# Kernel tuning notes

Measured on AMD Instinct MI355X. Metric: run time of the kernel, lower is better.

Reference implementation:

```python
import jax, jax.numpy as jnp
import numpy as np

D_MODEL = 2048
NUM_Q_HEADS = 32
NUM_KV_HEADS = 8
HEAD_DIM = D_MODEL // NUM_Q_HEADS  # 64
NUM_GROUPS = NUM_Q_HEADS // NUM_KV_HEADS  # 4
SCALE = float(np.sqrt(HEAD_DIM))


def setup_inputs() -> dict:
    key = jax.random.key(0)
    ks = jax.random.split(key, 5)
    B, S = 2, 2048
    std = 1.0 / np.sqrt(D_MODEL)
    return {
        "x": jax.random.normal(ks[0], (B, S, D_MODEL), dtype=jnp.float32),
        "W_q": jax.random.normal(ks[1], (D_MODEL, NUM_Q_HEADS * HEAD_DIM), dtype=jnp.float32) * std,
        "W_k": jax.random.normal(ks[2], (D_MODEL, NUM_KV_HEADS * HEAD_DIM), dtype=jnp.float32) * std,
        "W_v": jax.random.normal(ks[3], (D_MODEL, NUM_KV_HEADS * HEAD_DIM), dtype=jnp.float32) * std,
        "W_o": jax.random.normal(ks[4], (D_MODEL, D_MODEL), dtype=jnp.float32) * std,
    }


def reference(x, W_q, W_k, W_v, W_o):
    B, S, _ = x.shape
    # projections; weights stored as (in, out) so y = x @ W
    Q = (x @ W_q).reshape(B, S, NUM_Q_HEADS, HEAD_DIM).transpose(0, 2, 1, 3)   # [B,Hq,S,d]
    K = (x @ W_k).reshape(B, S, NUM_KV_HEADS, HEAD_DIM).transpose(0, 2, 1, 3)  # [B,Hkv,S,d]
    V = (x @ W_v).reshape(B, S, NUM_KV_HEADS, HEAD_DIM).transpose(0, 2, 1, 3)
    # repeat_interleave KV heads across groups (faithful to the original)
    K = jnp.repeat(K, NUM_GROUPS, axis=1)  # [B,Hq,S,d]
    V = jnp.repeat(V, NUM_GROUPS, axis=1)
    scores = jnp.einsum("bhqd,bhkd->bhqk", Q, K) / SCALE  # [B,Hq,S,S]
    attn = jax.nn.softmax(scores, axis=-1)
    out = jnp.einsum("bhqk,bhkd->bhqd", attn, V)  # [B,Hq,S,d]
    out = out.transpose(0, 2, 1, 3).reshape(B, S, D_MODEL)
    return out @ W_o
```

## Files before the change

### kernel.cpp

```cpp
#include <hip/hip_runtime.h>
#include <hip/hip_bf16.h>

#define D_MODEL 2048
#define NQH 32
#define NKVH 8
#define HD 64
#define SEQ 2048
#define BATCH 2
#define MTOT (BATCH * SEQ)

typedef __attribute__((ext_vector_type(8))) short short8;
typedef __attribute__((ext_vector_type(4))) float floatx4;
typedef __attribute__((ext_vector_type(16))) float f32x16;

#define QSCALE 0.18033688011112042f

static __device__ inline unsigned cvtpk(float lo, float hi) {
  unsigned r;
  asm("v_cvt_pk_bf16_f32 %0, %1, %2" : "=v"(r) : "v"(lo), "v"(hi));
  return r;
}
#define PLSWAP(a, b) asm("v_permlane32_swap_b32 %0, %1" : "+v"(a), "+v"(b))

__device__ inline void gload_lds16(const __hip_bfloat16* g, short* lds) {
  __builtin_amdgcn_global_load_lds(
      (const __attribute__((address_space(1))) void*)g,
      (__attribute__((address_space(3))) void*)lds, 16, 0, 0);
}

__global__ __launch_bounds__(256) void convx_k(const float* __restrict__ x,
                                               __hip_bfloat16* __restrict__ xb,
                                               int n4) {
  int i = blockIdx.x * 256 + threadIdx.x;
  int stride = gridDim.x * 256;
  for (; i < n4; i += stride) {
    float4 v = reinterpret_cast<const float4*>(x)[i];
    union { __hip_bfloat16 h[4]; uint2 u; } cv;
    cv.h[0] = __float2bfloat16(v.x);
    cv.h[1] = __float2bfloat16(v.y);
    cv.h[2] = __float2bfloat16(v.z);
    cv.h[3] = __float2bfloat16(v.w);
    reinterpret_cast<uint2*>(xb)[i] = cv.u;
  }
}

__global__ __launch_bounds__(256) void transw_k(const float* __restrict__ W,
                                                __hip_bfloat16* __restrict__ Wt,
                                                int Kd, int Nd) {
  __shared__ float t[32][33];
  int n0 = blockIdx.x * 32, k0 = blockIdx.y * 32;
  int tx = threadIdx.x, ty = threadIdx.y;
#pragma unroll
  for (int j = 0; j < 32; j += 8)
    t[ty + j][tx] = W[(size_t)(k0 + ty + j) * Nd + n0 + tx];
  __syncthreads();
#pragma unroll
  for (int j = 0; j < 32; j += 8)
    Wt[(size_t)(n0 + ty + j) * Kd + k0 + tx] = __float2bfloat16(t[tx][ty + j]);
}

template <int MODE>
__global__ __launch_bounds__(256) void gemm_bt_k(
    const __hip_bfloat16* __restrict__ A,
    const __hip_bfloat16* __restrict__ B0,
    const __hip_bfloat16* __restrict__ B1,
    const __hip_bfloat16* __restrict__ B2,
    float* __restrict__ Cf,
    __hip_bfloat16* __restrict__ O0,
    __hip_bfloat16* __restrict__ O1,
    __hip_bfloat16* __restrict__ O2) {
  constexpr int Kd = D_MODEL;
  __shared__ short As[128 * 32];
  __shared__ short Bs[128 * 32];

  const int tid = threadIdx.x;
  const int m0 = blockIdx.y * 128;
  const int n0 = blockIdx.x * 128;

  const __hip_bfloat16* Bt;
  if (MODE == 0) {
    Bt = B0 + (size_t)n0 * Kd;
  } else {
    if (n0 < 2048) Bt = B0 + (size_t)n0 * Kd;
    else if (n0 < 2560) Bt = B1 + (size_t)(n0 - 2048) * Kd;
    else Bt = B2 + (size_t)(n0 - 2560) * Kd;
  }
  const __hip_bfloat16* Ab = A + (size_t)m0 * Kd;

  const int w = tid >> 6, l = tid & 63;
  const int wr = w >> 1, wc = w & 1;
  const int lc = l & 15, l4 = l >> 4;

  const int srow = w * 32 + (l >> 2);
  const int scol = (l & 3) * 8;
  const __hip_bfloat16* ga = Ab + (size_t)srow * Kd + scol;
  const __hip_bfloat16* gb = Bt + (size_t)srow * Kd + scol;
  short* la0 = &As[(w * 32) * 32];
  short* la1 = &As[(w * 32 + 16) * 32];
  short* lb0 = &Bs[(w * 32) * 32];
  short* lb1 = &Bs[(w * 32 + 16) * 32];

  floatx4 acc[4][4] = {};

  for (int kt = 0; kt < Kd; kt += 32) {
    gload_lds16(ga + kt, la0);
    gload_lds16(ga + (size_t)16 * Kd + kt, la1);
    gload_lds16(gb + kt, lb0);
    gload_lds16(gb + (size_t)16 * Kd + kt, lb1);
    __syncthreads();

    short8 af[4], bf[4];
#pragma unroll
    for (int mi = 0; mi < 4; ++mi)
      af[mi] = *reinterpret_cast<const short8*>(&As[(wr * 64 + mi * 16 + lc) * 32 + l4 * 8]);
#pragma unroll
    for (int ni = 0; ni < 4; ++ni)
      bf[ni] = *reinterpret_cast<const short8*>(&Bs[(wc * 64 + ni * 16 + lc) * 32 + l4 * 8]);
#pragma unroll
    for (int mi = 0; mi < 4; ++mi)
#pragma unroll
      for (int ni = 0; ni < 4; ++ni)
        acc[mi][ni] = __builtin_amdgcn_mfma_f32_16x16x32_bf16(af[mi], bf[ni], acc[mi][ni], 0, 0, 0);
    __syncthreads();
  }

#pragma unroll
  for (int mi = 0; mi < 4; ++mi)
#pragma unroll
    for (int ni = 0; ni < 4; ++ni)
#pragma unroll
      for (int i = 0; i < 4; ++i) {
        int m = m0 + wr * 64 + mi * 16 + l4 * 4 + i;
        int ncol = n0 + wc * 64 + ni * 16 + lc;
        float v = acc[mi][ni][i];
        if (MODE == 0) {
          Cf[(size_t)m * 2048 + ncol] = v;
        } else {
          int bb = m >> 11, s = m & 2047;
          if (ncol < 2048) {
            int hh = ncol >> 6, dd = ncol & 63;
            O0[(((size_t)bb * NQH + hh) * SEQ + s) * HD + dd] = __float2bfloat16(v * QSCALE);
          } else if (ncol < 2560) {
            int c2 = ncol - 2048;
            int hh = c2 >> 6, dd = c2 & 63;
            O1[(((size_t)bb * NKVH + hh) * SEQ + s) * HD + dd] = __float2bfloat16(v);
          } else {
            int c2 = ncol - 2560;
            int hh = c2 >> 6, dd = c2 & 63;
            O2[(((size_t)bb * NKVH + hh) * HD + dd) * SEQ + s] = __float2bfloat16(v);
          }
        }
      }
}

__global__ __launch_bounds__(256, 2) void attn_k(const __hip_bfloat16* __restrict__ Qb,
                                                 const __hip_bfloat16* __restrict__ Kb,
                                                 const __hip_bfloat16* __restrict__ Vtb,
                                                 __hip_bfloat16* __restrict__ Ao) {
  __shared__ short Ks[2][64 * 64];
  __shared__ short Vs[2][64 * 64];
  __shared__ float Ls[4][64];

  const int bid = blockIdx.x;
  const int xcd = bid & 7, j = bid >> 3;
  const int g = xcd * 2 + (j >> 5), wv = j & 31;
  const int b = g >> 3, kh = g & 7;
  const int h = kh * 4 + (wv >> 3), qt = wv & 7;

  const int tid = threadIdx.x, w = tid >> 6, l = tid & 63;
  const int q5 = l & 31, hl = l >> 5;

  const __hip_bfloat16* Qp = Qb + (((size_t)b * NQH + h) * SEQ + qt * 256 + w * 64) * HD;
  const __hip_bfloat16* Kp = Kb + ((size_t)b * NKVH + kh) * SEQ * HD;
  const __hip_bfloat16* Vp = Vtb + ((size_t)b * NKVH + kh) * HD * SEQ;

  short8 qf[2][4];
#pragma unroll
  for (int qb_ = 0; qb_ < 2; ++qb_)
#pragma unroll
    for (int ks = 0; ks < 4; ++ks)
      qf[qb_][ks] = *reinterpret_cast<const short8*>(
          Qp + (size_t)(qb_ * 32 + q5) * HD + ks * 16 + hl * 8);

  f32x16 acc[2][2] = {};
  float lsum[2] = {0.f, 0.f};

  const int sr = w * 8 + (l >> 3);
  const int sc = (l & 7) ^ (sr & 7);

  gload_lds16(Kp + (size_t)sr * HD + sc * 8, &Ks[0][w * 512]);
  gload_lds16(Kp + (size_t)(sr + 32) * HD + sc * 8, &Ks[0][2048 + w * 512]);
  gload_lds16(Vp + (size_t)sr * SEQ + sc * 8, &Vs[0][w * 512]);
  gload_lds16(Vp + (size_t)(sr + 32) * SEQ + sc * 8, &Vs[0][2048 + w * 512]);
  __syncthreads();

  int buf = 0;
  for (int kb = 0; kb < SEQ / 64; ++kb) {
    if (kb < SEQ / 64 - 1) {
      const __hip_bfloat16* Kn = Kp + (size_t)(kb + 1) * 64 * HD;
      const __hip_bfloat16* Vn = Vp + (size_t)(kb + 1) * 64;
      gload_lds16(Kn + (size_t)sr * HD + sc * 8, &Ks[buf ^ 1][w * 512]);
      gload_lds16(Kn + (size_t)(sr + 32) * HD + sc * 8, &Ks[buf ^ 1][2048 + w * 512]);
      gload_lds16(Vn + (size_t)sr * SEQ + sc * 8, &Vs[buf ^ 1][w * 512]);
      gload_lds16(Vn + (size_t)(sr + 32) * SEQ + sc * 8, &Vs[buf ^ 1][2048 + w * 512]);
    }

    const short* Kt = Ks[buf];
    const short* Vt = Vs[buf];

    short8 kf[2][4], vf[2][4];
#pragma unroll
    for (int kblk = 0; kblk < 2; ++kblk)
#pragma unroll
      for (int ks = 0; ks < 4; ++ks) {
        int row = kblk * 32 + q5;
        int ch = (ks * 2 + hl) ^ (row & 7);
        kf[kblk][ks] = *reinterpret_cast<const short8*>(Kt + row * 64 + ch * 8);
      }
#pragma unroll
    for (int db = 0; db < 2; ++db)
#pragma unroll
      for (int t = 0; t < 4; ++t) {
        int row = db * 32 + q5;
        int ch = (t * 2 + hl) ^ (row & 7);
        vf[db][t] = *reinterpret_cast<const short8*>(Vt + row * 64 + ch * 8);
      }

#pragma unroll
    for (int qb_ = 0; qb_ < 2; ++qb_) {
      f32x16 st0 = {}, st1 = {};
      __builtin_amdgcn_s_setprio(1);
#pragma unroll
      for (int ks = 0; ks < 4; ++ks) {
        st0 = __builtin_amdgcn_mfma_f32_32x32x16_bf16(kf[0][ks], qf[qb_][ks], st0, 0, 0, 0);
        st1 = __builtin_amdgcn_mfma_f32_32x32x16_bf16(kf[1][ks], qf[qb_][ks], st1, 0, 0, 0);
      }
      __builtin_amdgcn_s_setprio(0);

      float ps = 0.f;
      unsigned u[2][8];
#pragma unroll
      for (int jj = 0; jj < 8; ++jj) {
        float e0 = exp2f(st0[2 * jj]), e1 = exp2f(st0[2 * jj + 1]);
        float f0 = exp2f(st1[2 * jj]), f1 = exp2f(st1[2 * jj + 1]);
        ps += (e0 + e1) + (f0 + f1);
        u[0][jj] = cvtpk(e0, e1);
        u[1][jj] = cvtpk(f0, f1);
      }
      lsum[qb_] += ps;

      PLSWAP(u[0][0], u[0][2]); PLSWAP(u[0][1], u[0][3]);
      PLSWAP(u[0][4], u[0][6]); PLSWAP(u[0][5], u[0][7]);
      PLSWAP(u[1][0], u[1][2]); PLSWAP(u[1][1], u[1][3]);
      PLSWAP(u[1][4], u[1][6]); PLSWAP(u[1][5], u[1][7]);

      __builtin_amdgcn_s_setprio(1);
#pragma unroll
      for (int t = 0; t < 4; ++t) {
        union { unsigned w4[4]; short8 s8; } pa;
        pa.w4[0] = u[t >> 1][(t & 1) * 4 + 0];
        pa.w4[1] = u[t >> 1][(t & 1) * 4 + 1];
        pa.w4[2] = u[t >> 1][(t & 1) * 4 + 2];
        pa.w4[3] = u[t >> 1][(t & 1) * 4 + 3];
        acc[qb_][0] = __builtin_amdgcn_mfma_f32_32x32x16_bf16(pa.s8, vf[0][t], acc[qb_][0], 0, 0, 0);
        acc[qb_][1] = __builtin_amdgcn_mfma_f32_32x32x16_bf16(pa.s8, vf[1][t], acc[qb_][1], 0, 0, 0);
      }
      __builtin_amdgcn_s_setprio(0);
    }
    __syncthreads();
    buf ^= 1;
  }

#pragma unroll
  for (int qb_ = 0; qb_ < 2; ++qb_) {
    float v = lsum[qb_];
    v += __shfl_xor(v, 32);
    if (l < 32) Ls[w][qb_ * 32 + l] = v;
  }
  __syncthreads();

  const size_t obase = (size_t)b * SEQ + qt * 256 + w * 64;
#pragma unroll
  for (int qb_ = 0; qb_ < 2; ++qb_) {
    float inv[16];
#pragma unroll
    for (int r = 0; r < 16; ++r)
      inv[r] = 1.0f / Ls[w][qb_ * 32 + (r & 3) + 8 * (r >> 2) + 4 * hl];
#pragma unroll
    for (int db = 0; db < 2; ++db)
#pragma unroll
      for (int r = 0; r < 16; ++r) {
        int q = qb_ * 32 + (r & 3) + 8 * (r >> 2) + 4 * hl;
        Ao[(obase + q) * D_MODEL + h * HD + db * 32 + q5] =
            __float2bfloat16(acc[qb_][db][r] * inv[r]);
      }
  }
}

extern "C" void kernel_launch(void* const* d_in, const int* in_sizes, int n_in,
                              void* d_out, int out_size, void* d_ws, size_t ws_size,
                              hipStream_t stream) {
  const float* x  = (const float*)d_in[0];
  const float* Wq = (const float*)d_in[1];
  const float* Wk = (const float*)d_in[2];
  const float* Wv = (const float*)d_in[3];
  const float* Wo = (const float*)d_in[4];
  float* out = (float*)d_out;

  __hip_bfloat16* p = (__hip_bfloat16*)d_ws;
  __hip_bfloat16* xb  = p;
  __hip_bfloat16* Wqt = xb  + (size_t)MTOT * D_MODEL;
  __hip_bfloat16* Wkt = Wqt + (size_t)D_MODEL * D_MODEL;
  __hip_bfloat16* Wvt = Wkt + (size_t)512 * D_MODEL;
  __hip_bfloat16* Wot = Wvt + (size_t)512 * D_MODEL;
  __hip_bfloat16* Qb  = Wot + (size_t)D_MODEL * D_MODEL;
  __hip_bfloat16* Kb  = Qb  + (size_t)MTOT * D_MODEL;
  __hip_bfloat16* Vtb = Kb  + (size_t)BATCH * NKVH * SEQ * HD;
  __hip_bfloat16* Ab  = Vtb + (size_t)BATCH * NKVH * SEQ * HD;

  convx_k<<<2048, 256, 0, stream>>>(x, xb, MTOT * D_MODEL / 4);
  transw_k<<<dim3(D_MODEL / 32, D_MODEL / 32), dim3(32, 8), 0, stream>>>(Wq, Wqt, D_MODEL, D_MODEL);
  transw_k<<<dim3(512 / 32, D_MODEL / 32), dim3(32, 8), 0, stream>>>(Wk, Wkt, D_MODEL, 512);
  transw_k<<<dim3(512 / 32, D_MODEL / 32), dim3(32, 8), 0, stream>>>(Wv, Wvt, D_MODEL, 512);
  transw_k<<<dim3(D_MODEL / 32, D_MODEL / 32), dim3(32, 8), 0, stream>>>(Wo, Wot, D_MODEL, D_MODEL);

  gemm_bt_k<1><<<dim3(24, MTOT / 128), 256, 0, stream>>>(xb, Wqt, Wkt, Wvt,
                                                         nullptr, Qb, Kb, Vtb);
  attn_k<<<dim3(512), 256, 0, stream>>>(Qb, Kb, Vtb, Ab);
  gemm_bt_k<0><<<dim3(D_MODEL / 128, MTOT / 128), 256, 0, stream>>>(Ab, Wot, nullptr, nullptr,
                                                                    out, nullptr, nullptr, nullptr);
}
```

Baseline: 255.1 us.

## Halve attention query tile per wave, double grid, raise occupancy, re-layout LDS

The attention kernel now gives each wave 32 query rows instead of 64. The grid doubles to 1024 blocks and launch bounds go from 2 to 4 blocks per CU, so more waves are available to hide latency. K/V tiles in LDS move from an XOR-swizzled row layout to a chunk-major layout, so fragment reads stay conflict-free without the swizzle. The next-tile prefetch and the V fragment loads are moved after the QK MFMAs and the exp work, to overlap them with compute. The cost is that each K/V tile is reused by half as many queries, which doubles K/V global and LDS traffic per unit of work, and the global loads are less coalesced.

```diff
diff --git a/kernel.cpp b/kernel.cpp
--- a/kernel.cpp
+++ b/kernel.cpp
@@ -153,147 +153,132 @@
       }
 }
 
-__global__ __launch_bounds__(256, 2) void attn_k(const __hip_bfloat16* __restrict__ Qb,
+__global__ __launch_bounds__(256, 4) void attn_k(const __hip_bfloat16* __restrict__ Qb,
                                                  const __hip_bfloat16* __restrict__ Kb,
                                                  const __hip_bfloat16* __restrict__ Vtb,
                                                  __hip_bfloat16* __restrict__ Ao) {
   __shared__ short Ks[2][64 * 64];
   __shared__ short Vs[2][64 * 64];
-  __shared__ float Ls[4][64];
+  __shared__ float Ls[4][32];
 
   const int bid = blockIdx.x;
   const int xcd = bid & 7, j = bid >> 3;
-  const int g = xcd * 2 + (j >> 5), wv = j & 31;
+  const int g = xcd * 2 + (j >> 6), wv = j & 63;
   const int b = g >> 3, kh = g & 7;
-  const int h = kh * 4 + (wv >> 3), qt = wv & 7;
+  const int h = kh * 4 + (wv >> 4), qt = wv & 15;
 
   const int tid = threadIdx.x, w = tid >> 6, l = tid & 63;
   const int q5 = l & 31, hl = l >> 5;
 
-  const __hip_bfloat16* Qp = Qb + (((size_t)b * NQH + h) * SEQ + qt * 256 + w * 64) * HD;
+  const __hip_bfloat16* Qp = Qb + (((size_t)b * NQH + h) * SEQ + qt * 128 + w * 32) * HD;
   const __hip_bfloat16* Kp = Kb + ((size_t)b * NKVH + kh) * SEQ * HD;
   const __hip_bfloat16* Vp = Vtb + ((size_t)b * NKVH + kh) * HD * SEQ;
 
-  short8 qf[2][4];
-#pragma unroll
-  for (int qb_ = 0; qb_ < 2; ++qb_)
-#pragma unroll
-    for (int ks = 0; ks < 4; ++ks)
-      qf[qb_][ks] = *reinterpret_cast<const short8*>(
-          Qp + (size_t)(qb_ * 32 + q5) * HD + ks * 16 + hl * 8);
-
-  f32x16 acc[2][2] = {};
-  float lsum[2] = {0.f, 0.f};
-
-  const int sr = w * 8 + (l >> 3);
-  const int sc = (l & 7) ^ (sr & 7);
-
-  gload_lds16(Kp + (size_t)sr * HD + sc * 8, &Ks[0][w * 512]);
-  gload_lds16(Kp + (size_t)(sr + 32) * HD + sc * 8, &Ks[0][2048 + w * 512]);
-  gload_lds16(Vp + (size_t)sr * SEQ + sc * 8, &Vs[0][w * 512]);
-  gload_lds16(Vp + (size_t)(sr + 32) * SEQ + sc * 8, &Vs[0][2048 + w * 512]);
+  short8 qf[4];
+#pragma unroll
+  for (int ks = 0; ks < 4; ++ks)
+    qf[ks] = *reinterpret_cast<const short8*>(Qp + (size_t)q5 * HD + ks * 16 + hl * 8);
+
+  f32x16 acc0 = {}, acc1 = {};
+  float lsum = 0.f;
+
+  const int c0 = 2 * w, c1 = 2 * w + 1;
+  const __hip_bfloat16* gK0 = Kp + (size_t)l * HD + c0 * 8;
+  const __hip_bfloat16* gK1 = Kp + (size_t)l * HD + c1 * 8;
+  const __hip_bfloat16* gV0 = Vp + (size_t)l * SEQ + c0 * 8;
+  const __hip_bfloat16* gV1 = Vp + (size_t)l * SEQ + c1 * 8;
+
+  gload_lds16(gK0, &Ks[0][c0 * 512]);
+  gload_lds16(gK1, &Ks[0][c1 * 512]);
+  gload_lds16(gV0, &Vs[0][c0 * 512]);
+  gload_lds16(gV1, &Vs[0][c1 * 512]);
   __syncthreads();
 
-  int buf = 0;
   for (int kb = 0; kb < SEQ / 64; ++kb) {
+    const short* Kt = Ks[kb & 1];
+    const short* Vt = Vs[kb & 1];
+    short* Kn = Ks[(kb & 1) ^ 1];
+    short* Vn = Vs[(kb & 1) ^ 1];
+
+    short8 kf0[4], kf1[4];
+#pragma unroll
+    for (int ks = 0; ks < 4; ++ks) {
+      kf0[ks] = *reinterpret_cast<const short8*>(Kt + ((ks * 2 + hl) * 64 + q5) * 8);
+      kf1[ks] = *reinterpret_cast<const short8*>(Kt + ((ks * 2 + hl) * 64 + 32 + q5) * 8);
+    }
+    f32x16 st0 = {}, st1 = {};
+    __builtin_amdgcn_s_setprio(1);
+#pragma unroll
+    for (int ks = 0; ks < 4; ++ks) {
+      st0 = __builtin_amdgcn_mfma_f32_32x32x16_bf16(kf0[ks], qf[ks], st0, 0, 0, 0);
+      st1 = __builtin_amdgcn_mfma_f32_32x32x16_bf16(kf1[ks], qf[ks], st1, 0, 0, 0);
+    }
+    __builtin_amdgcn_s_setprio(0);
+
     if (kb < SEQ / 64 - 1) {
-      const __hip_bfloat16* Kn = Kp + (size_t)(kb + 1) * 64 * HD;
-      const __hip_bfloat16* Vn = Vp + (size_t)(kb + 1) * 64;
-      gload_lds16(Kn + (size_t)sr * HD + sc * 8, &Ks[buf ^ 1][w * 512]);
-      gload_lds16(Kn + (size_t)(sr + 32) * HD + sc * 8, &Ks[buf ^ 1][2048 + w * 512]);
-      gload_lds16(Vn + (size_t)sr * SEQ + sc * 8, &Vs[buf ^ 1][w * 512]);
-      gload_lds16(Vn + (size_t)(sr + 32) * SEQ + sc * 8, &Vs[buf ^ 1][2048 + w * 512]);
-    }
-
-    const short* Kt = Ks[buf];
-    const short* Vt = Vs[buf];
-
-    short8 kf[2][4], vf[2][4];
-#pragma unroll
-    for (int kblk = 0; kblk < 2; ++kblk)
-#pragma unroll
-      for (int ks = 0; ks < 4; ++ks) {
-        int row = kblk * 32 + q5;
-        int ch = (ks * 2 + hl) ^ (row & 7);
-        kf[kblk][ks] = *reinterpret_cast<const short8*>(Kt + row * 64 + ch * 8);
-      }
-#pragma unroll
-    for (int db = 0; db < 2; ++db)
-#pragma unroll
-      for (int t = 0; t < 4; ++t) {
-        int row = db * 32 + q5;
-        int ch = (t * 2 + hl) ^ (row & 7);
-        vf[db][t] = *reinterpret_cast<const short8*>(Vt + row * 64 + ch * 8);
-      }
-
-#pragma unroll
-    for (int qb_ = 0; qb_ < 2; ++qb_) {
-      f32x16 st0 = {}, st1 = {};
-      __builtin_amdgcn_s_setprio(1);
-#pragma unroll
-      for (int ks = 0; ks < 4; ++ks) {
-        st0 = __builtin_amdgcn_mfma_f32_32x32x16_bf16(kf[0][ks], qf[qb_][ks], st0, 0, 0, 0);
-        st1 = __builtin_amdgcn_mfma_f32_32x32x16_bf16(kf[1][ks], qf[qb_][ks], st1, 0, 0, 0);
-      }
-      __builtin_amdgcn_s_setprio(0);
-
-      float ps = 0.f;
-      unsigned u[2][8];
-#pragma unroll
-      for (int jj = 0; jj < 8; ++jj) {
-        float e0 = exp2f(st0[2 * jj]), e1 = exp2f(st0[2 * jj + 1]);
-        float f0 = exp2f(st1[2 * jj]), f1 = exp2f(st1[2 * jj + 1]);
-        ps += (e0 + e1) + (f0 + f1);
-        u[0][jj] = cvtpk(e0, e1);
-        u[1][jj] = cvtpk(f0, f1);
-      }
-      lsum[qb_] += ps;
-
-      PLSWAP(u[0][0], u[0][2]); PLSWAP(u[0][1], u[0][3]);
-      PLSWAP(u[0][4], u[0][6]); PLSWAP(u[0][5], u[0][7]);
-      PLSWAP(u[1][0], u[1][2]); PLSWAP(u[1][1], u[1][3]);
-      PLSWAP(u[1][4], u[1][6]); PLSWAP(u[1][5], u[1][7]);
-
-      __builtin_amdgcn_s_setprio(1);
-#pragma unroll
-      for (int t = 0; t < 4; ++t) {
-        union { unsigned w4[4]; short8 s8; } pa;
-        pa.w4[0] = u[t >> 1][(t & 1) * 4 + 0];
-        pa.w4[1] = u[t >> 1][(t & 1) * 4 + 1];
-        pa.w4[2] = u[t >> 1][(t & 1) * 4 + 2];
-        pa.w4[3] = u[t >> 1][(t & 1) * 4 + 3];
-        acc[qb_][0] = __builtin_amdgcn_mfma_f32_32x32x16_bf16(pa.s8, vf[0][t], acc[qb_][0], 0, 0, 0);
-        acc[qb_][1] = __builtin_amdgcn_mfma_f32_32x32x16_bf16(pa.s8, vf[1][t], acc[qb_][1], 0, 0, 0);
-      }
-      __builtin_amdgcn_s_setprio(0);
-    }
+      gK0 += 64 * HD; gK1 += 64 * HD; gV0 += 64; gV1 += 64;
+      gload_lds16(gK0, &Kn[c0 * 512]);
+      gload_lds16(gK1, &Kn[c1 * 512]);
+      gload_lds16(gV0, &Vn[c0 * 512]);
+      gload_lds16(gV1, &Vn[c1 * 512]);
+    }
+
+    float ps = 0.f;
+    unsigned u0[8], u1[8];
+#pragma unroll
+    for (int jj = 0; jj < 8; ++jj) {
+      float e0 = exp2f(st0[2 * jj]), e1 = exp2f(st0[2 * jj + 1]);
+      float f0 = exp2f(st1[2 * jj]), f1 = exp2f(st1[2 * jj + 1]);
+      ps += (e0 + e1) + (f0 + f1);
+      u0[jj] = cvtpk(e0, e1);
+      u1[jj] = cvtpk(f0, f1);
+    }
+    lsum += ps;
+
+    short8 vf0[4], vf1[4];
+#pragma unroll
+    for (int t = 0; t < 4; ++t) {
+      vf0[t] = *reinterpret_cast<const short8*>(Vt + ((t * 2 + hl) * 64 + q5) * 8);
+      vf1[t] = *reinterpret_cast<const short8*>(Vt + ((t * 2 + hl) * 64 + 32 + q5) * 8);
+    }
+
+    PLSWAP(u0[0], u0[2]); PLSWAP(u0[1], u0[3]);
+    PLSWAP(u0[4], u0[6]); PLSWAP(u0[5], u0[7]);
+    PLSWAP(u1[0], u1[2]); PLSWAP(u1[1], u1[3]);
+    PLSWAP(u1[4], u1[6]); PLSWAP(u1[5], u1[7]);
+
+    __builtin_amdgcn_s_setprio(1);
+#pragma unroll
+    for (int t = 0; t < 4; ++t) {
+      union { unsigned w4[4]; short8 s8; } pa;
+      pa.w4[0] = (t >> 1 ? u1 : u0)[(t & 1) * 4 + 0];
+      pa.w4[1] = (t >> 1 ? u1 : u0)[(t & 1) * 4 + 1];
+      pa.w4[2] = (t >> 1 ? u1 : u0)[(t & 1) * 4 + 2];
+      pa.w4[3] = (t >> 1 ? u1 : u0)[(t & 1) * 4 + 3];
+      acc0 = __builtin_amdgcn_mfma_f32_32x32x16_bf16(pa.s8, vf0[t], acc0, 0, 0, 0);
+      acc1 = __builtin_amdgcn_mfma_f32_32x32x16_bf16(pa.s8, vf1[t], acc1, 0, 0, 0);
+    }
+    __builtin_amdgcn_s_setprio(0);
     __syncthreads();
-    buf ^= 1;
-  }
-
-#pragma unroll
-  for (int qb_ = 0; qb_ < 2; ++qb_) {
-    float v = lsum[qb_];
+  }
+
+  {
+    float v = lsum;
     v += __shfl_xor(v, 32);
-    if (l < 32) Ls[w][qb_ * 32 + l] = v;
+    if (l < 32) Ls[w][l] = v;
   }
   __syncthreads();
 
-  const size_t obase = (size_t)b * SEQ + qt * 256 + w * 64;
-#pragma unroll
-  for (int qb_ = 0; qb_ < 2; ++qb_) {
-    float inv[16];
-#pragma unroll
-    for (int r = 0; r < 16; ++r)
-      inv[r] = 1.0f / Ls[w][qb_ * 32 + (r & 3) + 8 * (r >> 2) + 4 * hl];
-#pragma unroll
-    for (int db = 0; db < 2; ++db)
-#pragma unroll
-      for (int r = 0; r < 16; ++r) {
-        int q = qb_ * 32 + (r & 3) + 8 * (r >> 2) + 4 * hl;
-        Ao[(obase + q) * D_MODEL + h * HD + db * 32 + q5] =
-            __float2bfloat16(acc[qb_][db][r] * inv[r]);
-      }
+  const size_t obase = (size_t)b * SEQ + qt * 128 + w * 32;
+  float inv[16];
+#pragma unroll
+  for (int r = 0; r < 16; ++r)
+    inv[r] = 1.0f / Ls[w][(r & 3) + 8 * (r >> 2) + 4 * hl];
+#pragma unroll
+  for (int r = 0; r < 16; ++r) {
+    int q = (r & 3) + 8 * (r >> 2) + 4 * hl;
+    Ao[(obase + q) * D_MODEL + h * HD + q5] = __float2bfloat16(acc0[r] * inv[r]);
+    Ao[(obase + q) * D_MODEL + h * HD + 32 + q5] = __float2bfloat16(acc1[r] * inv[r]);
   }
 }
 
@@ -326,7 +311,7 @@
 
   gemm_bt_k<1><<<dim3(24, MTOT / 128), 256, 0, stream>>>(xb, Wqt, Wkt, Wvt,
                                                          nullptr, Qb, Kb, Vtb);
-  attn_k<<<dim3(512), 256, 0, stream>>>(Qb, Kb, Vtb, Ab);
+  attn_k<<<dim3(1024), 256, 0, stream>>>(Qb, Kb, Vtb, Ab);
   gemm_bt_k<0><<<dim3(D_MODEL / 128, MTOT / 128), 256, 0, stream>>>(Ab, Wot, nullptr, nullptr,
                                                                     out, nullptr, nullptr, nullptr);
 }
```

Result: no change. 252.4 us (-1.0%).
